# Performance work log

Measured on AMD Instinct MI355X. Metric: run time of the kernel, lower is better.

## Reference

```python
import jax, jax.numpy as jnp
import numpy as np

DIM = 64
HID = 512
BATCH = 8192
W_SCALE = 0.05  # keeps alpha small so exp(alpha) stays stable over 64 sequential steps


def _build_masks(dim, hid, seed=0):
    # Faithful to MADE.create_masks: degrees m[-1]=m[1]=arange(dim), m[0]=randint(0,dim-1,hid)
    rng = np.random.RandomState(seed)
    m_in = np.arange(dim)
    m0 = rng.randint(0, dim - 1, size=hid)
    mask1 = (m_in[:, None] <= m0[None, :]).T.astype(np.float32)          # [hid, dim]
    base = (m0[:, None] < m_in[None, :]).T                               # [dim, hid]
    mask2 = np.repeat(base, 2, axis=0).astype(np.float32)                # [2*dim, hid]
    return mask1, mask2


def setup_inputs() -> dict:
    key = jax.random.key(0)
    kz, kw1, kb1, kw2, kb2 = jax.random.split(key, 5)
    mask1, mask2 = _build_masks(DIM, HID)
    return {
        "z": jax.random.normal(kz, (BATCH, DIM), dtype=jnp.float32),
        "W1": jax.random.normal(kw1, (HID, DIM), dtype=jnp.float32) * W_SCALE,
        "b1": jax.random.normal(kb1, (HID,), dtype=jnp.float32) * W_SCALE,
        "W2": jax.random.normal(kw2, (2 * DIM, HID), dtype=jnp.float32) * W_SCALE,
        "b2": jax.random.normal(kb2, (2 * DIM,), dtype=jnp.float32) * W_SCALE,
        "mask1": jnp.asarray(mask1),
        "mask2": jnp.asarray(mask2),
    }


def _made(x, W1, b1, W2, b2, mask1, mask2):
    # MaskedLinear: linear(x, mask*W, b); two layers with ReLU between
    h = jax.nn.relu(x @ (mask1 * W1).T + b1)      # [B, hid]
    return h @ (mask2 * W2).T + b2                # [B, 2*dim] -> chunk: mu=[:dim], alpha=[dim:]


def reference(z, W1, b1, W2, b2, mask1, mask2):
    dim = z.shape[1]

    def step(x, i):
        params = _made(x, W1, b1, W2, b2, mask1, mask2)
        mu_i = params[:, i]            # mu = params[:, :dim]
        alpha_i = params[:, dim + i]   # alpha = params[:, dim:]
        x = x.at[:, i].set(z[:, i] * jnp.exp(alpha_i) + mu_i)
        return x, None

    x, _ = jax.lax.scan(step, jnp.zeros_like(z), jnp.arange(dim))
    final_params = _made(x, W1, b1, W2, b2, mask1, mask2)
    log_det_jacobian = jnp.sum(final_params[:, dim:], axis=1)
    return x, log_det_jacobian
```

## Files before the change

### kernel.cpp

```cpp
#include <hip/hip_runtime.h>
#include <math.h>

#define DIM   64
#define HID   512
#define BATCH 8192
#define R     4

#define W1T_OFF   0
#define W2M_OFF   (DIM * HID)
#define W2SUM_OFF (W2M_OFF + 2 * DIM * HID)
#define B2SUM_OFF (W2SUM_OFF + HID)
#define WS_FLOATS (B2SUM_OFF + 1)

__global__ void prep_kernel(const float* __restrict__ W1,
                            const float* __restrict__ mask1,
                            const float* __restrict__ W2,
                            const float* __restrict__ mask2,
                            const float* __restrict__ b2,
                            float* __restrict__ ws) {
    int t = blockIdx.x * blockDim.x + threadIdx.x;
    const int n1 = DIM * HID;
    const int n2 = 2 * DIM * HID;
    if (t < n1) {
        int i = t / HID;
        int j = t - i * HID;
        ws[W1T_OFF + t] = mask1[j * DIM + i] * W1[j * DIM + i];
    } else if (t < n1 + n2) {
        int u = t - n1;
        ws[W2M_OFF + u] = mask2[u] * W2[u];
    } else if (t < n1 + n2 + HID) {
        int j = t - n1 - n2;
        float s = 0.f;
        for (int r = 0; r < DIM; ++r) {
            int idx = (DIM + r) * HID + j;
            s += mask2[idx] * W2[idx];
        }
        ws[W2SUM_OFF + j] = s;
    } else if (t == n1 + n2 + HID) {
        float s = 0.f;
        for (int r = 0; r < DIM; ++r) s += b2[DIM + r];
        ws[B2SUM_OFF] = s;
    }
}

__device__ __forceinline__ float wave_sum_dpp(float x) {
    x += __int_as_float(__builtin_amdgcn_update_dpp(0, __float_as_int(x), 0x111, 0xf, 0xf, true));
    x += __int_as_float(__builtin_amdgcn_update_dpp(0, __float_as_int(x), 0x112, 0xf, 0xf, true));
    x += __int_as_float(__builtin_amdgcn_update_dpp(0, __float_as_int(x), 0x114, 0xf, 0xf, true));
    x += __int_as_float(__builtin_amdgcn_update_dpp(0, __float_as_int(x), 0x118, 0xf, 0xf, true));
    x += __int_as_float(__builtin_amdgcn_update_dpp(0, __float_as_int(x), 0x142, 0xa, 0xf, true));
    x += __int_as_float(__builtin_amdgcn_update_dpp(0, __float_as_int(x), 0x143, 0xc, 0xf, true));
    return x;
}

__device__ __forceinline__ float readlane_f(float v, int lane) {
    return __int_as_float(__builtin_amdgcn_readlane(__float_as_int(v), lane));
}

__global__ __launch_bounds__(256, 2) void maf_kernel(
    const float* __restrict__ z,
    const float* __restrict__ b1,
    const float* __restrict__ b2,
    const float* __restrict__ ws,
    float* __restrict__ out) {
    const int lane = threadIdx.x & 63;
    const int wid  = (blockIdx.x * blockDim.x + threadIdx.x) >> 6;
    const int b0   = wid * R;

    const float* __restrict__ W1T = ws + W1T_OFF;
    const float* __restrict__ W2M = ws + W2M_OFF;
    const float* __restrict__ w2s = ws + W2SUM_OFF;

    float h[R][8];
    {
        const float4* bp = (const float4*)(b1 + lane * 8);
        float4 bv0 = bp[0], bv1 = bp[1];
#pragma unroll
        for (int r = 0; r < R; ++r) {
            h[r][0] = bv0.x; h[r][1] = bv0.y; h[r][2] = bv0.z; h[r][3] = bv0.w;
            h[r][4] = bv1.x; h[r][5] = bv1.y; h[r][6] = bv1.z; h[r][7] = bv1.w;
        }
    }
    float zl[R];
#pragma unroll
    for (int r = 0; r < R; ++r) zl[r] = z[(b0 + r) * DIM + lane];
    const float b2lo = b2[lane];
    const float b2hi = b2[DIM + lane];
    float xm[R] = {0.f, 0.f, 0.f, 0.f};

#define LOADW(i, m0, m1, a0, a1, c0, c1)                                   \
    do {                                                                   \
        const float4* _pm = (const float4*)(W2M + (i) * HID + lane * 8);   \
        const float4* _pa = (const float4*)(W2M + ((i) + DIM) * HID + lane * 8); \
        const float4* _pc = (const float4*)(W1T + (i) * HID + lane * 8);   \
        m0 = _pm[0]; m1 = _pm[1];                                          \
        a0 = _pa[0]; a1 = _pa[1];                                          \
        c0 = _pc[0]; c1 = _pc[1];                                          \
    } while (0)

#define STEP(i, m0, m1, a0, a1, c0, c1)                                    \
    do {                                                                   \
        float _pmv[R], _pav[R];                                            \
        _Pragma("unroll")                                                  \
        for (int r = 0; r < R; ++r) {                                      \
            float rh0 = fmaxf(h[r][0], 0.f), rh1 = fmaxf(h[r][1], 0.f);    \
            float rh2 = fmaxf(h[r][2], 0.f), rh3 = fmaxf(h[r][3], 0.f);    \
            float rh4 = fmaxf(h[r][4], 0.f), rh5 = fmaxf(h[r][5], 0.f);    \
            float rh6 = fmaxf(h[r][6], 0.f), rh7 = fmaxf(h[r][7], 0.f);    \
            float pm = rh0 * m0.x + rh1 * m0.y + rh2 * m0.z + rh3 * m0.w   \
                     + rh4 * m1.x + rh5 * m1.y + rh6 * m1.z + rh7 * m1.w;  \
            float pa = rh0 * a0.x + rh1 * a0.y + rh2 * a0.z + rh3 * a0.w   \
                     + rh4 * a1.x + rh5 * a1.y + rh6 * a1.z + rh7 * a1.w;  \
            _pmv[r] = wave_sum_dpp(pm);                                    \
            _pav[r] = wave_sum_dpp(pa);                                    \
        }                                                                  \
        const float _b2i  = readlane_f(b2lo, (i));                         \
        const float _b2di = readlane_f(b2hi, (i));                         \
        _Pragma("unroll")                                                  \
        for (int r = 0; r < R; ++r) {                                      \
            const float _zi = readlane_f(zl[r], (i));                      \
            float _xv = _zi * __expf(_pav[r] + _b2di) + (_pmv[r] + _b2i);  \
            const float _xs = readlane_f(_xv, 63);                         \
            if (lane == (i)) xm[r] = _xs;                                  \
            h[r][0] += _xs * c0.x; h[r][1] += _xs * c0.y;                  \
            h[r][2] += _xs * c0.z; h[r][3] += _xs * c0.w;                  \
            h[r][4] += _xs * c1.x; h[r][5] += _xs * c1.y;                  \
            h[r][6] += _xs * c1.z; h[r][7] += _xs * c1.w;                  \
        }                                                                  \
    } while (0)

    float4 m0A, m1A, a0A, a1A, c0A, c1A;
    float4 m0B, m1B, a0B, a1B, c0B, c1B;
    LOADW(0, m0A, m1A, a0A, a1A, c0A, c1A);

#pragma unroll 1
    for (int i = 0; i < DIM; i += 2) {
        LOADW(i + 1, m0B, m1B, a0B, a1B, c0B, c1B);
        __builtin_amdgcn_s_barrier();
        STEP(i, m0A, m1A, a0A, a1A, c0A, c1A);
        LOADW((i + 2) & 63, m0A, m1A, a0A, a1A, c0A, c1A);
        STEP(i + 1, m0B, m1B, a0B, a1B, c0B, c1B);
    }

    const float4* sp = (const float4*)(w2s + lane * 8);
    float4 s0 = sp[0], s1 = sp[1];
    const float bsum = ws[B2SUM_OFF];
#pragma unroll
    for (int r = 0; r < R; ++r) {
        out[(b0 + r) * DIM + lane] = xm[r];
        float pl = fmaxf(h[r][0], 0.f) * s0.x + fmaxf(h[r][1], 0.f) * s0.y
                 + fmaxf(h[r][2], 0.f) * s0.z + fmaxf(h[r][3], 0.f) * s0.w
                 + fmaxf(h[r][4], 0.f) * s1.x + fmaxf(h[r][5], 0.f) * s1.y
                 + fmaxf(h[r][6], 0.f) * s1.z + fmaxf(h[r][7], 0.f) * s1.w;
        pl = wave_sum_dpp(pl);
        if (lane == 63) out[BATCH * DIM + b0 + r] = pl + bsum;
    }
#undef LOADW
#undef STEP
}

extern "C" void kernel_launch(void* const* d_in, const int* in_sizes, int n_in,
                              void* d_out, int out_size, void* d_ws, size_t ws_size,
                              hipStream_t stream) {
    const float* z     = (const float*)d_in[0];
    const float* W1    = (const float*)d_in[1];
    const float* b1    = (const float*)d_in[2];
    const float* W2    = (const float*)d_in[3];
    const float* b2    = (const float*)d_in[4];
    const float* mask1 = (const float*)d_in[5];
    const float* mask2 = (const float*)d_in[6];
    float* out = (float*)d_out;
    float* ws  = (float*)d_ws;

    {
        int total  = WS_FLOATS;
        int blocks = (total + 255) / 256;
        prep_kernel<<<blocks, 256, 0, stream>>>(W1, mask1, W2, mask2, b2, ws);
    }
    {
        int threads = 256;
        int blocks  = BATCH / (R * 4);
        maf_kernel<<<blocks, threads, 0, stream>>>(z, b1, b2, ws, out);
    }
}
```

Measured before the change: 73.38 us.

## Interleave per-step weights into records, halve rows per wave, use packed vector math

Repacks the masked W2 mu row, W2 alpha row and transposed W1 column for each step into one contiguous 1536-float record, so each step's weight loads come from a single advancing pointer. It also cuts rows per wave from 4 to 2, which doubles the wave count, and raises launch bounds to 4 blocks per CU to increase occupancy. Per-row math is rewritten with 4-wide vector types so the compiler can emit packed FMA and max instructions. The last two steps are peeled out of the loop to drop the wraparound prefetch. The cost is that each weight load is now shared by fewer rows, so total weight traffic from cache doubles.

```diff
diff --git a/kernel.cpp b/kernel.cpp
--- a/kernel.cpp
+++ b/kernel.cpp
@@ -4,13 +4,15 @@
 #define DIM   64
 #define HID   512
 #define BATCH 8192
-#define R     4
+#define R     2
+#define REC   1536
 
-#define W1T_OFF   0
-#define W2M_OFF   (DIM * HID)
-#define W2SUM_OFF (W2M_OFF + 2 * DIM * HID)
+#define W2SUM_OFF (64 * REC)
 #define B2SUM_OFF (W2SUM_OFF + HID)
 #define WS_FLOATS (B2SUM_OFF + 1)
+
+typedef float f32x4 __attribute__((ext_vector_type(4)));
+typedef float f32x2 __attribute__((ext_vector_type(2)));
 
 __global__ void prep_kernel(const float* __restrict__ W1,
                             const float* __restrict__ mask1,
@@ -19,24 +21,31 @@
                             const float* __restrict__ b2,
                             float* __restrict__ ws) {
     int t = blockIdx.x * blockDim.x + threadIdx.x;
-    const int n1 = DIM * HID;
-    const int n2 = 2 * DIM * HID;
-    if (t < n1) {
-        int i = t / HID;
-        int j = t - i * HID;
-        ws[W1T_OFF + t] = mask1[j * DIM + i] * W1[j * DIM + i];
-    } else if (t < n1 + n2) {
-        int u = t - n1;
-        ws[W2M_OFF + u] = mask2[u] * W2[u];
-    } else if (t < n1 + n2 + HID) {
-        int j = t - n1 - n2;
+    const int nrec = 64 * REC;
+    if (t < nrec) {
+        int rec = t / REC;
+        int pos = t - rec * REC;
+        float v;
+        if (pos < HID) {
+            int j = pos;
+            v = mask2[rec * HID + j] * W2[rec * HID + j];
+        } else if (pos < 2 * HID) {
+            int j = pos - HID;
+            v = mask2[(DIM + rec) * HID + j] * W2[(DIM + rec) * HID + j];
+        } else {
+            int j = pos - 2 * HID;
+            v = mask1[j * DIM + rec] * W1[j * DIM + rec];
+        }
+        ws[t] = v;
+    } else if (t < nrec + HID) {
+        int j = t - nrec;
         float s = 0.f;
         for (int r = 0; r < DIM; ++r) {
             int idx = (DIM + r) * HID + j;
             s += mask2[idx] * W2[idx];
         }
         ws[W2SUM_OFF + j] = s;
-    } else if (t == n1 + n2 + HID) {
+    } else if (t == nrec + HID) {
         float s = 0.f;
         for (int r = 0; r < DIM; ++r) s += b2[DIM + r];
         ws[B2SUM_OFF] = s;
@@ -57,7 +66,7 @@
     return __int_as_float(__builtin_amdgcn_readlane(__float_as_int(v), lane));
 }
 
-__global__ __launch_bounds__(256, 2) void maf_kernel(
+__global__ __launch_bounds__(256, 4) void maf_kernel(
     const float* __restrict__ z,
     const float* __restrict__ b1,
     const float* __restrict__ b2,
@@ -66,93 +75,94 @@
     const int lane = threadIdx.x & 63;
     const int wid  = (blockIdx.x * blockDim.x + threadIdx.x) >> 6;
     const int b0   = wid * R;
+    const f32x4 Z4 = {0.f, 0.f, 0.f, 0.f};
 
-    const float* __restrict__ W1T = ws + W1T_OFF;
-    const float* __restrict__ W2M = ws + W2M_OFF;
-    const float* __restrict__ w2s = ws + W2SUM_OFF;
-
-    float h[R][8];
+    f32x4 h[R][2];
     {
-        const float4* bp = (const float4*)(b1 + lane * 8);
-        float4 bv0 = bp[0], bv1 = bp[1];
+        f32x4 bv0 = *(const f32x4*)(b1 + lane * 8);
+        f32x4 bv1 = *(const f32x4*)(b1 + lane * 8 + 4);
 #pragma unroll
-        for (int r = 0; r < R; ++r) {
-            h[r][0] = bv0.x; h[r][1] = bv0.y; h[r][2] = bv0.z; h[r][3] = bv0.w;
-            h[r][4] = bv1.x; h[r][5] = bv1.y; h[r][6] = bv1.z; h[r][7] = bv1.w;
-        }
+        for (int r = 0; r < R; ++r) { h[r][0] = bv0; h[r][1] = bv1; }
     }
     float zl[R];
 #pragma unroll
     for (int r = 0; r < R; ++r) zl[r] = z[(b0 + r) * DIM + lane];
     const float b2lo = b2[lane];
     const float b2hi = b2[DIM + lane];
-    float xm[R] = {0.f, 0.f, 0.f, 0.f};
+    float xm[R];
+#pragma unroll
+    for (int r = 0; r < R; ++r) xm[r] = 0.f;
 
-#define LOADW(i, m0, m1, a0, a1, c0, c1)                                   \
-    do {                                                                   \
-        const float4* _pm = (const float4*)(W2M + (i) * HID + lane * 8);   \
-        const float4* _pa = (const float4*)(W2M + ((i) + DIM) * HID + lane * 8); \
-        const float4* _pc = (const float4*)(W1T + (i) * HID + lane * 8);   \
-        m0 = _pm[0]; m1 = _pm[1];                                          \
-        a0 = _pa[0]; a1 = _pa[1];                                          \
-        c0 = _pc[0]; c1 = _pc[1];                                          \
+#define LOADW(p, M0, M1, A0, A1, C0, C1)                                    \
+    do {                                                                    \
+        M0 = *(const f32x4*)((p) - 512); M1 = *(const f32x4*)((p) - 508);   \
+        A0 = *(const f32x4*)(p);         A1 = *(const f32x4*)((p) + 4);     \
+        C0 = *(const f32x4*)((p) + 512); C1 = *(const f32x4*)((p) + 516);   \
     } while (0)
 
-#define STEP(i, m0, m1, a0, a1, c0, c1)                                    \
-    do {                                                                   \
-        float _pmv[R], _pav[R];                                            \
-        _Pragma("unroll")                                                  \
-        for (int r = 0; r < R; ++r) {                                      \
-            float rh0 = fmaxf(h[r][0], 0.f), rh1 = fmaxf(h[r][1], 0.f);    \
-            float rh2 = fmaxf(h[r][2], 0.f), rh3 = fmaxf(h[r][3], 0.f);    \
-            float rh4 = fmaxf(h[r][4], 0.f), rh5 = fmaxf(h[r][5], 0.f);    \
-            float rh6 = fmaxf(h[r][6], 0.f), rh7 = fmaxf(h[r][7], 0.f);    \
-            float pm = rh0 * m0.x + rh1 * m0.y + rh2 * m0.z + rh3 * m0.w   \
-                     + rh4 * m1.x + rh5 * m1.y + rh6 * m1.z + rh7 * m1.w;  \
-            float pa = rh0 * a0.x + rh1 * a0.y + rh2 * a0.z + rh3 * a0.w   \
-                     + rh4 * a1.x + rh5 * a1.y + rh6 * a1.z + rh7 * a1.w;  \
-            _pmv[r] = wave_sum_dpp(pm);                                    \
-            _pav[r] = wave_sum_dpp(pa);                                    \
-        }                                                                  \
-        const float _b2i  = readlane_f(b2lo, (i));                         \
-        const float _b2di = readlane_f(b2hi, (i));                         \
-        _Pragma("unroll")                                                  \
-        for (int r = 0; r < R; ++r) {                                      \
-            const float _zi = readlane_f(zl[r], (i));                      \
-            float _xv = _zi * __expf(_pav[r] + _b2di) + (_pmv[r] + _b2i);  \
-            const float _xs = readlane_f(_xv, 63);                         \
-            if (lane == (i)) xm[r] = _xs;                                  \
-            h[r][0] += _xs * c0.x; h[r][1] += _xs * c0.y;                  \
-            h[r][2] += _xs * c0.z; h[r][3] += _xs * c0.w;                  \
-            h[r][4] += _xs * c1.x; h[r][5] += _xs * c1.y;                  \
-            h[r][6] += _xs * c1.z; h[r][7] += _xs * c1.w;                  \
-        }                                                                  \
+#define STEP(i, M0, M1, A0, A1, C0, C1)                                     \
+    do {                                                                    \
+        float _pm[R], _pa[R];                                               \
+        _Pragma("unroll")                                                   \
+        for (int r = 0; r < R; ++r) {                                       \
+            f32x4 r0 = __builtin_elementwise_max(h[r][0], Z4);              \
+            f32x4 r1 = __builtin_elementwise_max(h[r][1], Z4);              \
+            f32x4 am = r0 * M0 + r1 * M1;                                   \
+            f32x4 aa = r0 * A0 + r1 * A1;                                   \
+            f32x2 tm = __builtin_shufflevector(am, am, 0, 1)                \
+                     + __builtin_shufflevector(am, am, 2, 3);               \
+            f32x2 ta = __builtin_shufflevector(aa, aa, 0, 1)                \
+                     + __builtin_shufflevector(aa, aa, 2, 3);               \
+            _pm[r] = wave_sum_dpp(tm.x + tm.y);                             \
+            _pa[r] = wave_sum_dpp(ta.x + ta.y);                             \
+        }                                                                   \
+        const float _b2i  = readlane_f(b2lo, (i));                          \
+        const float _b2di = readlane_f(b2hi, (i));                          \
+        const bool  _at   = (lane == (i));                                  \
+        _Pragma("unroll")                                                   \
+        for (int r = 0; r < R; ++r) {                                       \
+            const float _zi = readlane_f(zl[r], (i));                       \
+            float _xv = _zi * __expf(_pa[r] + _b2di) + (_pm[r] + _b2i);     \
+            const float _xs = readlane_f(_xv, 63);                          \
+            if (_at) xm[r] = _xs;                                           \
+            h[r][0] += C0 * _xs;                                            \
+            h[r][1] += C1 * _xs;                                            \
+        }                                                                   \
     } while (0)
 
-    float4 m0A, m1A, a0A, a1A, c0A, c1A;
-    float4 m0B, m1B, a0B, a1B, c0B, c1B;
-    LOADW(0, m0A, m1A, a0A, a1A, c0A, c1A);
+    f32x4 m0A, m1A, a0A, a1A, c0A, c1A;
+    f32x4 m0B, m1B, a0B, a1B, c0B, c1B;
+
+    const float* wp = ws + HID + lane * 8;
+    LOADW(wp, m0A, m1A, a0A, a1A, c0A, c1A);
+    wp += REC;
 
 #pragma unroll 1
-    for (int i = 0; i < DIM; i += 2) {
-        LOADW(i + 1, m0B, m1B, a0B, a1B, c0B, c1B);
+    for (int i = 0; i < 62; i += 2) {
+        LOADW(wp, m0B, m1B, a0B, a1B, c0B, c1B);
         __builtin_amdgcn_s_barrier();
         STEP(i, m0A, m1A, a0A, a1A, c0A, c1A);
-        LOADW((i + 2) & 63, m0A, m1A, a0A, a1A, c0A, c1A);
+        const float* wq = wp + REC;
+        LOADW(wq, m0A, m1A, a0A, a1A, c0A, c1A);
         STEP(i + 1, m0B, m1B, a0B, a1B, c0B, c1B);
+        wp = wq + REC;
     }
+    LOADW(wp, m0B, m1B, a0B, a1B, c0B, c1B);
+    STEP(62, m0A, m1A, a0A, a1A, c0A, c1A);
+    STEP(63, m0B, m1B, a0B, a1B, c0B, c1B);
 
-    const float4* sp = (const float4*)(w2s + lane * 8);
-    float4 s0 = sp[0], s1 = sp[1];
+    const float* w2s = ws + W2SUM_OFF;
+    f32x4 s0 = *(const f32x4*)(w2s + lane * 8);
+    f32x4 s1 = *(const f32x4*)(w2s + lane * 8 + 4);
     const float bsum = ws[B2SUM_OFF];
 #pragma unroll
     for (int r = 0; r < R; ++r) {
         out[(b0 + r) * DIM + lane] = xm[r];
-        float pl = fmaxf(h[r][0], 0.f) * s0.x + fmaxf(h[r][1], 0.f) * s0.y
-                 + fmaxf(h[r][2], 0.f) * s0.z + fmaxf(h[r][3], 0.f) * s0.w
-                 + fmaxf(h[r][4], 0.f) * s1.x + fmaxf(h[r][5], 0.f) * s1.y
-                 + fmaxf(h[r][6], 0.f) * s1.z + fmaxf(h[r][7], 0.f) * s1.w;
-        pl = wave_sum_dpp(pl);
+        f32x4 acc = __builtin_elementwise_max(h[r][0], Z4) * s0
+                  + __builtin_elementwise_max(h[r][1], Z4) * s1;
+        f32x2 t = __builtin_shufflevector(acc, acc, 0, 1)
+                + __builtin_shufflevector(acc, acc, 2, 3);
+        float pl = wave_sum_dpp(t.x + t.y);
         if (lane == 63) out[BATCH * DIM + b0 + r] = pl + bsum;
     }
 #undef LOADW
```

Result: slower. 75.74 us (+3.2%).
